# Kernel optimization log

Measured on AMD Instinct MI355X. Metric: run time of the kernel, lower is better.

The kernel has to match this reference:

```python
import jax, jax.numpy as jnp
import numpy as np

B, T = 1, 1024
HID = 2048
H, HKV, D = 16, 4, 128
G = H // HKV          # kv groups
TOPK = 256
HI, DI = 4, 32        # indexer heads / head dim


def _rotate_half(x):
    x1, x2 = jnp.split(x, 2, axis=-1)
    return jnp.concatenate([-x2, x1], axis=-1)


def _apply_rotary(x, cos, sin):
    # x: (B,T,H,D), cos/sin: (1,T,1,D)
    return x * cos + _rotate_half(x) * sin


def _rms_norm(x):
    eps = jnp.finfo(x.dtype).eps
    return x * jax.lax.rsqrt(jnp.mean(x * x, axis=-1, keepdims=True) + eps)


def setup_inputs() -> dict:
    key = jax.random.key(0)
    ks = jax.random.split(key, 9)
    s = 0.02
    x = jax.random.normal(ks[0], (B, T, HID), jnp.float32)
    # rotary tables
    inv_freq = 1.0 / (10000.0 ** (jnp.arange(0, D, 2, dtype=jnp.float32) / D))
    freqs = jnp.outer(jnp.arange(T, dtype=jnp.float32), inv_freq)   # (T, D/2)
    emb = jnp.concatenate([freqs, freqs], axis=-1)                  # (T, D)
    cos = jnp.cos(emb)[None, :, None, :]
    sin = jnp.sin(emb)[None, :, None, :]
    Wq = jax.random.normal(ks[1], (HID, H * D), jnp.float32) * s
    Wk = jax.random.normal(ks[2], (HID, HKV * D), jnp.float32) * s
    Wv = jax.random.normal(ks[3], (HID, HKV * D), jnp.float32) * s
    Wo = jax.random.normal(ks[4], (H * D, HID), jnp.float32) * s
    Wqi = jax.random.normal(ks[5], (HID, HI * DI), jnp.float32) * s
    Wwi = jax.random.normal(ks[6], (HID, HI), jnp.float32) * s
    Wki = jax.random.normal(ks[7], (HID, DI), jnp.float32) * s
    return {"x": x, "cos": cos, "sin": sin, "Wq": Wq, "Wk": Wk, "Wv": Wv,
            "Wo": Wo, "Wqi": Wqi, "Wwi": Wwi, "Wki": Wki}


def reference(x, cos, sin, Wq, Wk, Wv, Wo, Wqi, Wwi, Wki):
    b, t, _ = x.shape
    q = (x @ Wq).reshape(b, t, H, D)
    k = (x @ Wk).reshape(b, t, HKV, D)
    v = (x @ Wv).reshape(b, t, HKV, D)
    q = _rms_norm(_apply_rotary(q, cos, sin))
    k = _rms_norm(_apply_rotary(k, cos, sin))

    # ---- lightning indexer: I[t,s] = sum_j w[t,j] * relu(q_i[t,j] . k_i[s]) ----
    qi = (x @ Wqi).reshape(b, t, HI, DI)
    wi = x @ Wwi                                   # (B,T,HI)
    ki = x @ Wki                                   # (B,T,DI)
    raw = jax.nn.relu(jnp.einsum('bthd,bsd->bths', qi, ki))
    idx_scores = jnp.einsum('bths,bth->bts', raw, wi)     # (B,T,T)

    pos = jnp.arange(t)
    causal = pos[None, :] <= pos[:, None]                 # (T,T) valid s<=t
    masked = jnp.where(causal[None], idx_scores, -jnp.inf)
    _, top_idx = jax.lax.top_k(masked, TOPK)              # (B,T,K) int32

    # gather selected K/V: (B,T,K,HKV,D)
    gather = jax.vmap(lambda arr, idx: arr[idx])          # per-batch fancy gather
    sel_k = gather(k, top_idx)
    sel_v = gather(v, top_idx)
    sel_mask = top_idx <= pos[None, :, None]              # (B,T,K)

    # grouped-query attention over selected tokens (avoid repeat_interleave)
    q5 = q.reshape(b, t, HKV, G, D)                       # q head h -> kv head h//G
    scale = D ** -0.5
    scores = jnp.einsum('btngd,btknd->btngk', q5, sel_k) * scale
    scores = jnp.where(sel_mask[:, :, None, None, :], scores, -jnp.inf)
    probs = jax.nn.softmax(scores, axis=-1)
    attn = jnp.einsum('btngk,btknd->btngd', probs, sel_v)  # (B,T,HKV,G,D)
    out = attn.reshape(b, t, H * D) @ Wo
    return out
```

## Files before the change

kernel.cpp:

```cpp
#include <hip/hip_runtime.h>
#include <hip/hip_bf16.h>
#include <math.h>

#define T_    1024
#define HID_  2048
#define NH    16
#define NKV   4
#define DH    128
#define TOPK_ 256
#define HI_   4
#define DI_   32
#define NPROJ 3072
#define NIDX  164
#define KSPLIT 8
#define KCHUNK 256

#ifndef INFINITY
#define INFINITY (__builtin_inff())
#endif

typedef __attribute__((ext_vector_type(8))) short bf16x8;
typedef __attribute__((ext_vector_type(4))) float f32x4;

__device__ inline unsigned int packbf(float f) {
    unsigned int u = __float_as_uint(f);
    return (u + 0x7fffu + ((u >> 16) & 1u)) >> 16;
}

#define GLDS16(g, l) __builtin_amdgcn_global_load_lds( \
    (const __attribute__((address_space(1))) void*)(g), \
    (__attribute__((address_space(3))) void*)(l), 16, 0, 0)

__device__ inline void tcast_body(const float* __restrict__ W, unsigned short* __restrict__ Wt,
                                  int N, int bx, int by, int tid, float (*tile)[33]) {
    const int n0 = bx * 32, k0 = by * 32;
    const int tx = tid & 31, ty = tid >> 5;
#pragma unroll
    for (int i = 0; i < 4; ++i)
        tile[ty + i * 8][tx] = W[(size_t)(k0 + ty + i * 8) * N + (n0 + tx)];
    __syncthreads();
#pragma unroll
    for (int i = 0; i < 4; ++i) {
        int n = n0 + ty + i * 8;
        Wt[(size_t)n * HID_ + k0 + tx] = (unsigned short)packbf(tile[tx][ty + i * 8]);
    }
}

__global__ __launch_bounds__(256) void prep1(const float* __restrict__ x,
                                             const float* __restrict__ Wq,
                                             const float* __restrict__ Wk,
                                             const float* __restrict__ Wv,
                                             const float* __restrict__ Wqi,
                                             const float* __restrict__ Wwi,
                                             const float* __restrict__ Wki,
                                             unsigned short* __restrict__ xb,
                                             unsigned short* __restrict__ WtAll,
                                             float* __restrict__ Wi) {
    __shared__ float tile[32][33];
    int bid = blockIdx.x;
    const int tid = threadIdx.x;
    if (bid < 4096) { tcast_body(Wq, WtAll, HID_, bid & 63, bid >> 6, tid, tile); return; }
    bid -= 4096;
    if (bid < 1024) { tcast_body(Wk, WtAll + (size_t)2048 * HID_, 512, bid & 15, bid >> 4, tid, tile); return; }
    bid -= 1024;
    if (bid < 1024) { tcast_body(Wv, WtAll + (size_t)2560 * HID_, 512, bid & 15, bid >> 4, tid, tile); return; }
    bid -= 1024;
    if (bid < 1024) {
        int e = bid * 256 + tid;
        const float4* p = (const float4*)(x + (size_t)e * 8);
        float4 a = p[0], b = p[1];
        uint4 r;
        r.x = packbf(a.x) | (packbf(a.y) << 16);
        r.y = packbf(a.z) | (packbf(a.w) << 16);
        r.z = packbf(b.x) | (packbf(b.y) << 16);
        r.w = packbf(b.z) | (packbf(b.w) << 16);
        *(uint4*)(xb + (size_t)e * 8) = r;
        return;
    }
    bid -= 1024;
    {
        int e = bid * 256 + tid;
        if (e >= HID_ * NIDX) return;
        int k = e / NIDX, c = e - k * NIDX;
        float v;
        if (c < 128) v = Wqi[(size_t)k * 128 + c];
        else if (c < 132) v = Wwi[(size_t)k * 4 + (c - 128)];
        else v = Wki[(size_t)k * 32 + (c - 132)];
        Wi[e] = v;
    }
}

__global__ void tcast(const float* __restrict__ W, unsigned short* __restrict__ Wt, int N) {
    __shared__ float tile[32][33];
    const int n0 = blockIdx.x * 32, k0 = blockIdx.y * 32;
    const int tx = threadIdx.x, ty = threadIdx.y;
#pragma unroll
    for (int i = 0; i < 4; ++i)
        tile[ty + i * 8][tx] = W[(size_t)(k0 + ty + i * 8) * N + (n0 + tx)];
    __syncthreads();
#pragma unroll
    for (int i = 0; i < 4; ++i) {
        int n = n0 + ty + i * 8;
        Wt[(size_t)n * HID_ + k0 + tx] = (unsigned short)packbf(tile[tx][ty + i * 8]);
    }
}

__global__ __launch_bounds__(256) void gemm64(const unsigned short* __restrict__ A,
                                              const unsigned short* __restrict__ Bt,
                                              float* __restrict__ C,
                                              int K, int ldc) {
    __shared__ unsigned short As[64 * 64];
    __shared__ unsigned short Bs[64 * 64];
    const int tid = threadIdx.x, lane = tid & 63, w = tid >> 6;
    const int wr = w >> 1, wc = w & 1;
    const int brow = blockIdx.y * 64, bcol = blockIdx.x * 64;
    const int l15 = lane & 15, lq = lane >> 4;

    f32x4 acc[2][2] = {};

    const int srow = tid >> 3;
    const int gsrc = ((tid & 7) ^ (srow & 7)) * 8;
    const unsigned short* ga  = A  + (size_t)(brow + srow) * K + gsrc;
    const unsigned short* ga2 = ga + (size_t)32 * K;
    const unsigned short* gb  = Bt + (size_t)(bcol + srow) * K + gsrc;
    const unsigned short* gb2 = gb + (size_t)32 * K;
    unsigned short* la  = &As[(size_t)tid * 8];
    unsigned short* la2 = &As[(size_t)(tid + 256) * 8];
    unsigned short* lb  = &Bs[(size_t)tid * 8];
    unsigned short* lb2 = &Bs[(size_t)(tid + 256) * 8];

    for (int k0 = 0; k0 < K; k0 += 64) {
        GLDS16(ga + k0,  la);
        GLDS16(ga2 + k0, la2);
        GLDS16(gb + k0,  lb);
        GLDS16(gb2 + k0, lb2);
        __syncthreads();
        bf16x8 fa[2][2], fb[2][2];
#pragma unroll
        for (int m = 0; m < 2; ++m)
#pragma unroll
            for (int kk = 0; kk < 2; ++kk) {
                int row = wr * 32 + m * 16 + l15;
                fa[m][kk] = *(const bf16x8*)&As[row * 64 + (((kk * 4 + lq) ^ (l15 & 7)) * 8)];
            }
#pragma unroll
        for (int nn = 0; nn < 2; ++nn)
#pragma unroll
            for (int kk = 0; kk < 2; ++kk) {
                int row = wc * 32 + nn * 16 + l15;
                fb[nn][kk] = *(const bf16x8*)&Bs[row * 64 + (((kk * 4 + lq) ^ (l15 & 7)) * 8)];
            }
#pragma unroll
        for (int kk = 0; kk < 2; ++kk)
#pragma unroll
            for (int m = 0; m < 2; ++m)
#pragma unroll
                for (int nn = 0; nn < 2; ++nn)
                    acc[m][nn] = __builtin_amdgcn_mfma_f32_16x16x32_bf16(fa[m][kk], fb[nn][kk], acc[m][nn], 0, 0, 0);
        __syncthreads();
    }
#pragma unroll
    for (int m = 0; m < 2; ++m)
#pragma unroll
        for (int nn = 0; nn < 2; ++nn)
#pragma unroll
            for (int q = 0; q < 4; ++q) {
                int row = brow + wr * 32 + m * 16 + lq * 4 + q;
                int col = bcol + wc * 32 + nn * 16 + l15;
                C[(size_t)row * ldc + col] = acc[m][nn][q];
            }
}

__global__ void gemm_f32_splitk(const float* __restrict__ A, const float* __restrict__ B,
                                float* __restrict__ Cpart, int M, int N, int K) {
    __shared__ float As2[16][64 + 1];
    __shared__ float Bs2[16][64 + 1];
    const int tid = threadIdx.x;
    const int tx = tid & 15, ty = tid >> 4;
    const int brow = blockIdx.y * 64, bcol = blockIdx.x * 64;
    const int z = blockIdx.z;
    const int kbeg = z * KCHUNK, kend = kbeg + KCHUNK;

    float acc[4][4];
#pragma unroll
    for (int i = 0; i < 4; ++i)
#pragma unroll
        for (int j = 0; j < 4; ++j) acc[i][j] = 0.f;

    for (int k0 = kbeg; k0 < kend; k0 += 16) {
#pragma unroll
        for (int it = 0; it < 4; ++it) {
            int i = tid + it * 256;
            int r = i >> 4, c = i & 15;
            As2[c][r] = A[(size_t)(brow + r) * K + (k0 + c)];
        }
#pragma unroll
        for (int it = 0; it < 4; ++it) {
            int i = tid + it * 256;
            int r = i >> 6, c = i & 63;
            int col = bcol + c;
            Bs2[r][c] = (col < N) ? B[(size_t)(k0 + r) * N + col] : 0.f;
        }
        __syncthreads();
#pragma unroll
        for (int kk = 0; kk < 16; ++kk) {
            float a[4], b[4];
#pragma unroll
            for (int i = 0; i < 4; ++i) a[i] = As2[kk][ty * 4 + i];
#pragma unroll
            for (int j = 0; j < 4; ++j) b[j] = Bs2[kk][tx * 4 + j];
#pragma unroll
            for (int i = 0; i < 4; ++i)
#pragma unroll
                for (int j = 0; j < 4; ++j) acc[i][j] += a[i] * b[j];
        }
        __syncthreads();
    }
#pragma unroll
    for (int i = 0; i < 4; ++i) {
        int r = brow + ty * 4 + i;
#pragma unroll
        for (int j = 0; j < 4; ++j) {
            int c = bcol + tx * 4 + j;
            if (c < N) Cpart[((size_t)z * M + r) * N + c] = acc[i][j];
        }
    }
}

__global__ __launch_bounds__(256) void reduce_k(const float* __restrict__ Cpart,
                                                float* __restrict__ Cout,
                                                float* __restrict__ kib, int MN) {
    int e = blockIdx.x * 256 + threadIdx.x;
    if (e >= MN) return;
    float s = 0.f;
#pragma unroll
    for (int z = 0; z < KSPLIT; ++z) s += Cpart[(size_t)z * MN + e];
    Cout[e] = s;
    int t = e / NIDX, c = e - t * NIDX;
    if (c >= 132) kib[(size_t)t * DI_ + (c - 132)] = s;
}

__global__ void rope_fused(const float* __restrict__ proj, const float* __restrict__ cosb,
                           const float* __restrict__ sinb, unsigned short* __restrict__ qbb,
                           unsigned short* __restrict__ kbb, unsigned int* __restrict__ vbb) {
    const int t = blockIdx.x, h = blockIdx.y, lane = threadIdx.x;
    if (h < 20) {
        const float* row;
        unsigned short* dst;
        if (h < 16) { row = proj + (size_t)t * NPROJ + h * DH;           dst = qbb + ((size_t)t * NH + h) * DH; }
        else        { row = proj + (size_t)t * NPROJ + HID_ + (h - 16) * DH; dst = kbb + ((size_t)t * NKV + (h - 16)) * DH; }
        float a = row[lane], b = row[lane + 64];
        float c0 = cosb[t * DH + lane],      s0 = sinb[t * DH + lane];
        float c1 = cosb[t * DH + lane + 64], s1 = sinb[t * DH + lane + 64];
        float r0 = a * c0 - b * s0;
        float r1 = b * c1 + a * s1;
        float ss = r0 * r0 + r1 * r1;
#pragma unroll
        for (int o = 32; o > 0; o >>= 1) ss += __shfl_xor(ss, o);
        float inv = rsqrtf(ss * (1.0f / 128.0f) + 1.1920929e-07f);
        dst[lane]      = (unsigned short)packbf(r0 * inv);
        dst[lane + 64] = (unsigned short)packbf(r1 * inv);
    } else {
        const float* src = proj + (size_t)t * NPROJ + HID_ + 512;
#pragma unroll
        for (int i = 0; i < 4; ++i) {
            int c2 = lane + i * 64;
            vbb[(size_t)t * 256 + c2] = packbf(src[2 * c2]) | (packbf(src[2 * c2 + 1]) << 16);
        }
    }
}

__global__ __launch_bounds__(256) void idxtopk(const float* __restrict__ proji,
                                               const float* __restrict__ kib,
                                               int* __restrict__ idxout) {
    const int t = blockIdx.x, tid = threadIdx.x;
    int* orow = idxout + (size_t)t * TOPK_;
    if (t < TOPK_) { orow[tid] = tid; return; }

    __shared__ float qsh[128];
    __shared__ float wsh[4];
    if (tid < 128) qsh[tid] = proji[(size_t)t * NIDX + tid];
    else if (tid < 132) wsh[tid - 128] = proji[(size_t)t * NIDX + tid];
    __syncthreads();

    const int n = t + 1;
    const int lane = tid & 63, wave = tid >> 6;

    unsigned int key[4];
#pragma unroll
    for (int j = 0; j < 4; ++j) {
        int s = j * 256 + tid;
        if (s < n) {
            const float4* kr = (const float4*)&kib[(size_t)s * DI_];
            float4 k4[8];
#pragma unroll
            for (int d4 = 0; d4 < 8; ++d4) k4[d4] = kr[d4];
            float sc = 0.f;
#pragma unroll
            for (int h = 0; h < HI_; ++h) {
                float d = 0.f;
#pragma unroll
                for (int d4 = 0; d4 < 8; ++d4) {
                    const float* qp = &qsh[h * 32 + d4 * 4];
                    d += k4[d4].x * qp[0] + k4[d4].y * qp[1] +
                         k4[d4].z * qp[2] + k4[d4].w * qp[3];
                }
                sc += wsh[h] * fmaxf(d, 0.f);
            }
            unsigned int u = __float_as_uint(sc);
            key[j] = (u & 0x80000000u) ? ~u : (u | 0x80000000u);
        } else key[j] = 0u;
    }

    __shared__ int wcnt[2][4];
    unsigned int prefix = 0;
#pragma unroll 1
    for (int b = 31; b >= 0; --b) {
        unsigned int cand = prefix | (1u << b);
        int c = (key[0] >= cand) + (key[1] >= cand) + (key[2] >= cand) + (key[3] >= cand);
#pragma unroll
        for (int o = 32; o > 0; o >>= 1) c += __shfl_xor(c, o);
        if (lane == 0) wcnt[b & 1][wave] = c;
        __syncthreads();
        int total = wcnt[b & 1][0] + wcnt[b & 1][1] + wcnt[b & 1][2] + wcnt[b & 1][3];
        if (total >= TOPK_) prefix = cand;
    }
    const unsigned int T = prefix;

    __shared__ int posc;
    __shared__ int eqtot[4][4];
    __syncthreads();
    {
        int c = (key[0] > T) + (key[1] > T) + (key[2] > T) + (key[3] > T);
#pragma unroll
        for (int o = 32; o > 0; o >>= 1) c += __shfl_xor(c, o);
        if (lane == 0) wcnt[0][wave] = c;
    }
    if (tid == 0) posc = 0;

    int e[4]; int myp[4];
#pragma unroll
    for (int j = 0; j < 4; ++j) {
        e[j] = (key[j] == T) ? 1 : 0;
        unsigned long long m = __ballot(e[j]);
        myp[j] = __popcll(m & ((1ull << lane) - 1ull));
        if (lane == 0) eqtot[j][wave] = __popcll(m);
    }
    __syncthreads();
    const int cntGT = wcnt[0][0] + wcnt[0][1] + wcnt[0][2] + wcnt[0][3];
    const int need = TOPK_ - cntGT;

#pragma unroll
    for (int j = 0; j < 4; ++j)
        if (key[j] > T) {
            int p = atomicAdd(&posc, 1);
            orow[p] = j * 256 + tid;
        }
    int runbase = 0;
#pragma unroll
    for (int j = 0; j < 4; ++j) {
        int wavebase = 0;
#pragma unroll
        for (int w2 = 0; w2 < 4; ++w2) if (w2 < wave) wavebase += eqtot[j][w2];
        int g = runbase + wavebase + myp[j];
        if (e[j] && g < need) orow[cntGT + g] = j * 256 + tid;
        runbase += eqtot[j][0] + eqtot[j][1] + eqtot[j][2] + eqtot[j][3];
    }
}

__global__ __launch_bounds__(256) void attn3(const unsigned short* __restrict__ qbb,
                                             const unsigned short* __restrict__ kbb,
                                             const unsigned short* __restrict__ vbb,
                                             const int* __restrict__ idx,
                                             unsigned short* __restrict__ attnb) {
    const int t = blockIdx.x, n = blockIdx.y;
    const int tid = threadIdx.x, lane = tid & 63, w = tid >> 6;
    const int C = (t + 1 < TOPK_) ? t + 1 : TOPK_;
    const int l15 = lane & 15, lq = lane >> 4;

    __shared__ int sidx[TOPK_];
    __shared__ float sp[4][TOPK_];
    __shared__ float sinv[4];
    __shared__ unsigned short P[16][264];
    __shared__ unsigned short Vs[64][136];

    sidx[tid] = idx[(size_t)t * TOPK_ + tid];
    __syncthreads();

    const size_t qrow = (size_t)t * NH + n * 4 + (l15 < 4 ? l15 : 3);
    bf16x8 qf[4];
#pragma unroll
    for (int ks = 0; ks < 4; ++ks)
        qf[ks] = *(const bf16x8*)&qbb[qrow * DH + ks * 32 + lq * 8];

#pragma unroll
    for (int tt = 0; tt < 4; ++tt) {
        const int tile = w * 4 + tt;
        const int tok = tile * 16 + l15;
        const unsigned short* krow = &kbb[((size_t)sidx[tok] * NKV + n) * DH];
        f32x4 acc = {0.f, 0.f, 0.f, 0.f};
        __builtin_amdgcn_s_setprio(1);
#pragma unroll
        for (int ks = 0; ks < 4; ++ks) {
            bf16x8 yf = *(const bf16x8*)&krow[ks * 32 + lq * 8];
            acc = __builtin_amdgcn_mfma_f32_16x16x32_bf16(qf[ks], yf, acc, 0, 0, 0);
        }
        __builtin_amdgcn_s_setprio(0);
        if (lane < 16) {
            int j = tile * 16 + lane;
            bool ok = j < C;
#pragma unroll
            for (int q = 0; q < 4; ++q)
                sp[q][j] = ok ? acc[q] * 0.08838834764831845f : -INFINITY;
        }
    }
    __syncthreads();

    {
        float v0 = sp[w][lane], v1 = sp[w][lane + 64],
              v2 = sp[w][lane + 128], v3 = sp[w][lane + 192];
        float m = fmaxf(fmaxf(v0, v1), fmaxf(v2, v3));
#pragma unroll
        for (int o = 32; o > 0; o >>= 1) m = fmaxf(m, __shfl_xor(m, o));
        float e0 = expf(v0 - m), e1 = expf(v1 - m), e2 = expf(v2 - m), e3 = expf(v3 - m);
        float sum = e0 + e1 + e2 + e3;
#pragma unroll
        for (int o = 32; o > 0; o >>= 1) sum += __shfl_xor(sum, o);
        if (lane == 0) sinv[w] = 1.f / sum;
        P[w][lane]       = (unsigned short)packbf(e0);
        P[w][lane + 64]  = (unsigned short)packbf(e1);
        P[w][lane + 128] = (unsigned short)packbf(e2);
        P[w][lane + 192] = (unsigned short)packbf(e3);
    }

    f32x4 pacc[2] = {};
#pragma unroll 1
    for (int tau = 0; tau < 4; ++tau) {
        __syncthreads();
#pragma unroll
        for (int it = 0; it < 4; ++it) {
            int c = tid + it * 256;
            int r = c >> 4, doff = (c & 15) * 8;
            int col = doff ^ (((r >> 3) & 3) << 4);
            *(uint4*)&Vs[r][col] =
                *(const uint4*)&vbb[((size_t)sidx[tau * 64 + r] * NKV + n) * DH + doff];
        }
        __syncthreads();
#pragma unroll
        for (int kk = 0; kk < 2; ++kk) {
            bf16x8 xf = *(const bf16x8*)&P[l15][tau * 64 + kk * 32 + lq * 8];
            const int colr0 = ((2 * w + 0) * 16 + l15) ^ (lq << 4);
            const int colr1 = ((2 * w + 1) * 16 + l15) ^ (lq << 4);
            bf16x8 yf0, yf1;
#pragma unroll
            for (int j = 0; j < 8; ++j) {
                yf0[j] = (short)Vs[kk * 32 + lq * 8 + j][colr0];
                yf1[j] = (short)Vs[kk * 32 + lq * 8 + j][colr1];
            }
            __builtin_amdgcn_s_setprio(1);
            pacc[0] = __builtin_amdgcn_mfma_f32_16x16x32_bf16(xf, yf0, pacc[0], 0, 0, 0);
            pacc[1] = __builtin_amdgcn_mfma_f32_16x16x32_bf16(xf, yf1, pacc[1], 0, 0, 0);
            __builtin_amdgcn_s_setprio(0);
        }
    }

    if (lane < 16) {
#pragma unroll
        for (int dt = 0; dt < 2; ++dt)
#pragma unroll
            for (int q = 0; q < 4; ++q)
                attnb[(size_t)(t * NH + n * 4 + q) * DH + (2 * w + dt) * 16 + l15] =
                    (unsigned short)packbf(pacc[dt][q] * sinv[q]);
    }
}

extern "C" void kernel_launch(void* const* d_in, const int* in_sizes, int n_in,
                              void* d_out, int out_size, void* d_ws, size_t ws_size,
                              hipStream_t stream) {
    const float* x    = (const float*)d_in[0];
    const float* cosb = (const float*)d_in[1];
    const float* sinb = (const float*)d_in[2];
    const float* Wq   = (const float*)d_in[3];
    const float* Wk   = (const float*)d_in[4];
    const float* Wv   = (const float*)d_in[5];
    const float* Wo   = (const float*)d_in[6];
    const float* Wqi  = (const float*)d_in[7];
    const float* Wwi  = (const float*)d_in[8];
    const float* Wki  = (const float*)d_in[9];
    float* out = (float*)d_out;

    unsigned short* xb    = (unsigned short*)d_ws;
    unsigned short* WtAll = xb + 2097152;
    float*  proj  = (float*)(WtAll + 6291456);
    float*  Wi    = proj + 3145728;
    float*  proji = Wi + 335872;
    float*  kib   = proji + 167936;
    int*    idxb  = (int*)(kib + 1048576);
    unsigned short* kbb   = (unsigned short*)(idxb + 262144);
    unsigned short* vbb   = kbb + 524288;
    unsigned short* attnb = vbb + 524288;
    unsigned short* Wot   = WtAll;
    unsigned short* qbb   = xb;
    float* Cpart = (float*)kbb;

    prep1<<<dim3(8480), dim3(256), 0, stream>>>(x, Wq, Wk, Wv, Wqi, Wwi, Wki, xb, WtAll, Wi);

    gemm64<<<dim3(NPROJ / 64, T_ / 64), dim3(256), 0, stream>>>(xb, WtAll, proj, HID_, NPROJ);
    gemm_f32_splitk<<<dim3((NIDX + 63) / 64, T_ / 64, KSPLIT), dim3(256), 0, stream>>>(x, Wi, Cpart, T_, NIDX, HID_);
    reduce_k<<<dim3((T_ * NIDX + 255) / 256), dim3(256), 0, stream>>>(Cpart, proji, kib, T_ * NIDX);

    tcast<<<dim3(64, 64), dim3(32, 8), 0, stream>>>(Wo, Wot, HID_);

    rope_fused<<<dim3(T_, 21), dim3(64), 0, stream>>>(proj, cosb, sinb, qbb, kbb, (unsigned int*)vbb);

    idxtopk<<<dim3(T_), dim3(256), 0, stream>>>(proji, kib, idxb);

    attn3<<<dim3(T_, NKV), dim3(256), 0, stream>>>(qbb, kbb, vbb, idxb, attnb);

    gemm64<<<dim3(HID_ / 64, T_ / 64), dim3(256), 0, stream>>>(attnb, Wot, out, HID_, HID_);
}
```

Measured before the change: 183.7 us.

## Merge independent kernels into two heterogeneous block-dispatched launches

Combines the bf16 projection GEMM and the fp32 split-K indexer GEMM into one launch that picks its role from the block id. It also merges the RoPE/RMSnorm conversion, the Wo transpose-cast and the indexer top-k into a second launch. This removes several kernel launches and lets independent work fill the GPU at the same time. In exchange, blocks with very different resource needs share one kernel, so shared-memory size and register use are the union of all branches, which may reduce occupancy. RoPE now packs four tokens-heads per 256-thread block.

After: 183.9 us. About the same (+0.1%).

```diff
diff --git a/kernel.cpp b/kernel.cpp
--- a/kernel.cpp
+++ b/kernel.cpp
@@ -44,6 +44,71 @@
         int n = n0 + ty + i * 8;
         Wt[(size_t)n * HID_ + k0 + tx] = (unsigned short)packbf(tile[tx][ty + i * 8]);
     }
+}
+
+__device__ inline void gemm64_body(const unsigned short* __restrict__ A,
+                                   const unsigned short* __restrict__ Bt,
+                                   float* __restrict__ C, int K, int ldc,
+                                   int bx, int by, int tid,
+                                   unsigned short* As, unsigned short* Bs) {
+    const int lane = tid & 63, w = tid >> 6;
+    const int wr = w >> 1, wc = w & 1;
+    const int brow = by * 64, bcol = bx * 64;
+    const int l15 = lane & 15, lq = lane >> 4;
+
+    f32x4 acc[2][2] = {};
+
+    const int srow = tid >> 3;
+    const int gsrc = ((tid & 7) ^ (srow & 7)) * 8;
+    const unsigned short* ga  = A  + (size_t)(brow + srow) * K + gsrc;
+    const unsigned short* ga2 = ga + (size_t)32 * K;
+    const unsigned short* gb  = Bt + (size_t)(bcol + srow) * K + gsrc;
+    const unsigned short* gb2 = gb + (size_t)32 * K;
+    unsigned short* la  = &As[(size_t)tid * 8];
+    unsigned short* la2 = &As[(size_t)(tid + 256) * 8];
+    unsigned short* lb  = &Bs[(size_t)tid * 8];
+    unsigned short* lb2 = &Bs[(size_t)(tid + 256) * 8];
+
+    for (int k0 = 0; k0 < K; k0 += 64) {
+        GLDS16(ga + k0,  la);
+        GLDS16(ga2 + k0, la2);
+        GLDS16(gb + k0,  lb);
+        GLDS16(gb2 + k0, lb2);
+        __syncthreads();
+        bf16x8 fa[2][2], fb[2][2];
+#pragma unroll
+        for (int m = 0; m < 2; ++m)
+#pragma unroll
+            for (int kk = 0; kk < 2; ++kk) {
+                int row = wr * 32 + m * 16 + l15;
+                fa[m][kk] = *(const bf16x8*)&As[row * 64 + (((kk * 4 + lq) ^ (l15 & 7)) * 8)];
+            }
+#pragma unroll
+        for (int nn = 0; nn < 2; ++nn)
+#pragma unroll
+            for (int kk = 0; kk < 2; ++kk) {
+                int row = wc * 32 + nn * 16 + l15;
+                fb[nn][kk] = *(const bf16x8*)&Bs[row * 64 + (((kk * 4 + lq) ^ (l15 & 7)) * 8)];
+            }
+#pragma unroll
+        for (int kk = 0; kk < 2; ++kk)
+#pragma unroll
+            for (int m = 0; m < 2; ++m)
+#pragma unroll
+                for (int nn = 0; nn < 2; ++nn)
+                    acc[m][nn] = __builtin_amdgcn_mfma_f32_16x16x32_bf16(fa[m][kk], fb[nn][kk], acc[m][nn], 0, 0, 0);
+        __syncthreads();
+    }
+#pragma unroll
+    for (int m = 0; m < 2; ++m)
+#pragma unroll
+        for (int nn = 0; nn < 2; ++nn)
+#pragma unroll
+            for (int q = 0; q < 4; ++q) {
+                int row = brow + wr * 32 + m * 16 + lq * 4 + q;
+                int col = bcol + wc * 32 + nn * 16 + l15;
+                C[(size_t)row * ldc + col] = acc[m][nn][q];
+            }
 }
 
 __global__ __launch_bounds__(256) void prep1(const float* __restrict__ x,
@@ -90,18 +155,234 @@
     }
 }
 
-__global__ void tcast(const float* __restrict__ W, unsigned short* __restrict__ Wt, int N) {
+__global__ __launch_bounds__(256) void fusedA(const unsigned short* __restrict__ xb,
+                                              const unsigned short* __restrict__ WtAll,
+                                              float* __restrict__ proj,
+                                              const float* __restrict__ x,
+                                              const float* __restrict__ Wi,
+                                              float* __restrict__ Cpart) {
+    __shared__ unsigned short As[64 * 64];
+    __shared__ unsigned short Bs[64 * 64];
+    __shared__ float As2[16][64 + 1];
+    __shared__ float Bs2[16][64 + 1];
+    const int tid = threadIdx.x;
+    int bid = blockIdx.x;
+
+    if (bid < 768) {
+        gemm64_body(xb, WtAll, proj, HID_, NPROJ, bid % 48, bid / 48, tid, As, Bs);
+        return;
+    }
+    int s = bid - 768;
+    const int bx = s % 3, by = (s / 3) % 16, z = s / 48;
+    const int tx = tid & 15, ty = tid >> 4;
+    const int brow = by * 64, bcol = bx * 64;
+    const int kbeg = z * KCHUNK, kend = kbeg + KCHUNK;
+    const int M = T_, N = NIDX, K = HID_;
+
+    float acc[4][4];
+#pragma unroll
+    for (int i = 0; i < 4; ++i)
+#pragma unroll
+        for (int j = 0; j < 4; ++j) acc[i][j] = 0.f;
+
+    for (int k0 = kbeg; k0 < kend; k0 += 16) {
+#pragma unroll
+        for (int it = 0; it < 4; ++it) {
+            int i = tid + it * 256;
+            int r = i >> 4, c = i & 15;
+            As2[c][r] = x[(size_t)(brow + r) * K + (k0 + c)];
+        }
+#pragma unroll
+        for (int it = 0; it < 4; ++it) {
+            int i = tid + it * 256;
+            int r = i >> 6, c = i & 63;
+            int col = bcol + c;
+            Bs2[r][c] = (col < N) ? Wi[(size_t)(k0 + r) * N + col] : 0.f;
+        }
+        __syncthreads();
+#pragma unroll
+        for (int kk = 0; kk < 16; ++kk) {
+            float a[4], b[4];
+#pragma unroll
+            for (int i = 0; i < 4; ++i) a[i] = As2[kk][ty * 4 + i];
+#pragma unroll
+            for (int j = 0; j < 4; ++j) b[j] = Bs2[kk][tx * 4 + j];
+#pragma unroll
+            for (int i = 0; i < 4; ++i)
+#pragma unroll
+                for (int j = 0; j < 4; ++j) acc[i][j] += a[i] * b[j];
+        }
+        __syncthreads();
+    }
+#pragma unroll
+    for (int i = 0; i < 4; ++i) {
+        int r = brow + ty * 4 + i;
+#pragma unroll
+        for (int j = 0; j < 4; ++j) {
+            int c = bcol + tx * 4 + j;
+            if (c < N) Cpart[((size_t)z * M + r) * N + c] = acc[i][j];
+        }
+    }
+}
+
+__global__ __launch_bounds__(256) void reduce_k(const float* __restrict__ Cpart,
+                                                float* __restrict__ Cout,
+                                                float* __restrict__ kib, int MN) {
+    int e = blockIdx.x * 256 + threadIdx.x;
+    if (e >= MN) return;
+    float s = 0.f;
+#pragma unroll
+    for (int z = 0; z < KSPLIT; ++z) s += Cpart[(size_t)z * MN + e];
+    Cout[e] = s;
+    int t = e / NIDX, c = e - t * NIDX;
+    if (c >= 132) kib[(size_t)t * DI_ + (c - 132)] = s;
+}
+
+__global__ __launch_bounds__(256) void fusedB(const float* __restrict__ proj,
+                                              const float* __restrict__ cosb,
+                                              const float* __restrict__ sinb,
+                                              unsigned short* __restrict__ qbb,
+                                              unsigned short* __restrict__ kbb,
+                                              unsigned int* __restrict__ vbb,
+                                              const float* __restrict__ Wo,
+                                              unsigned short* __restrict__ Wot,
+                                              const float* __restrict__ proji,
+                                              const float* __restrict__ kib,
+                                              int* __restrict__ idxout) {
     __shared__ float tile[32][33];
-    const int n0 = blockIdx.x * 32, k0 = blockIdx.y * 32;
-    const int tx = threadIdx.x, ty = threadIdx.y;
-#pragma unroll
-    for (int i = 0; i < 4; ++i)
-        tile[ty + i * 8][tx] = W[(size_t)(k0 + ty + i * 8) * N + (n0 + tx)];
-    __syncthreads();
-#pragma unroll
-    for (int i = 0; i < 4; ++i) {
-        int n = n0 + ty + i * 8;
-        Wt[(size_t)n * HID_ + k0 + tx] = (unsigned short)packbf(tile[tx][ty + i * 8]);
+    const int tid = threadIdx.x;
+    int bid = blockIdx.x;
+
+    if (bid < 5376) {
+        const int w = tid >> 6, lane = tid & 63;
+        const int u = bid * 4 + w;
+        const int t = u / 21, h = u - t * 21;
+        if (h < 20) {
+            const float* row;
+            unsigned short* dst;
+            if (h < 16) { row = proj + (size_t)t * NPROJ + h * DH;               dst = qbb + ((size_t)t * NH + h) * DH; }
+            else        { row = proj + (size_t)t * NPROJ + HID_ + (h - 16) * DH; dst = kbb + ((size_t)t * NKV + (h - 16)) * DH; }
+            float a = row[lane], b = row[lane + 64];
+            float c0 = cosb[t * DH + lane],      s0 = sinb[t * DH + lane];
+            float c1 = cosb[t * DH + lane + 64], s1 = sinb[t * DH + lane + 64];
+            float r0 = a * c0 - b * s0;
+            float r1 = b * c1 + a * s1;
+            float ss = r0 * r0 + r1 * r1;
+#pragma unroll
+            for (int o = 32; o > 0; o >>= 1) ss += __shfl_xor(ss, o);
+            float inv = rsqrtf(ss * (1.0f / 128.0f) + 1.1920929e-07f);
+            dst[lane]      = (unsigned short)packbf(r0 * inv);
+            dst[lane + 64] = (unsigned short)packbf(r1 * inv);
+        } else {
+            const float* src = proj + (size_t)t * NPROJ + HID_ + 512;
+#pragma unroll
+            for (int i = 0; i < 4; ++i) {
+                int c2 = lane + i * 64;
+                vbb[(size_t)t * 256 + c2] = packbf(src[2 * c2]) | (packbf(src[2 * c2 + 1]) << 16);
+            }
+        }
+        return;
+    }
+    bid -= 5376;
+    if (bid < 4096) {
+        tcast_body(Wo, Wot, HID_, bid & 63, bid >> 6, tid, tile);
+        return;
+    }
+    bid -= 4096;
+    {
+        const int t = bid;
+        int* orow = idxout + (size_t)t * TOPK_;
+        if (t < TOPK_) { orow[tid] = tid; return; }
+
+        __shared__ float qsh[128];
+        __shared__ float wsh[4];
+        if (tid < 128) qsh[tid] = proji[(size_t)t * NIDX + tid];
+        else if (tid < 132) wsh[tid - 128] = proji[(size_t)t * NIDX + tid];
+        __syncthreads();
+
+        const int n = t + 1;
+        const int lane = tid & 63, wave = tid >> 6;
+
+        unsigned int key[4];
+#pragma unroll
+        for (int j = 0; j < 4; ++j) {
+            int s = j * 256 + tid;
+            if (s < n) {
+                const float4* kr = (const float4*)&kib[(size_t)s * DI_];
+                float4 k4[8];
+#pragma unroll
+                for (int d4 = 0; d4 < 8; ++d4) k4[d4] = kr[d4];
+                float sc = 0.f;
+#pragma unroll
+                for (int h = 0; h < HI_; ++h) {
+                    float d = 0.f;
+#pragma unroll
+                    for (int d4 = 0; d4 < 8; ++d4) {
+                        const float* qp = &qsh[h * 32 + d4 * 4];
+                        d += k4[d4].x * qp[0] + k4[d4].y * qp[1] +
+                             k4[d4].z * qp[2] + k4[d4].w * qp[3];
+                    }
+                    sc += wsh[h] * fmaxf(d, 0.f);
+                }
+                unsigned int u = __float_as_uint(sc);
+                key[j] = (u & 0x80000000u) ? ~u : (u | 0x80000000u);
+            } else key[j] = 0u;
+        }
+
+        __shared__ int wcnt[2][4];
+        unsigned int prefix = 0;
+#pragma unroll 1
+        for (int b = 31; b >= 0; --b) {
+            unsigned int cand = prefix | (1u << b);
+            int c = (key[0] >= cand) + (key[1] >= cand) + (key[2] >= cand) + (key[3] >= cand);
+#pragma unroll
+            for (int o = 32; o > 0; o >>= 1) c += __shfl_xor(c, o);
+            if (lane == 0) wcnt[b & 1][wave] = c;
+            __syncthreads();
+            int total = wcnt[b & 1][0] + wcnt[b & 1][1] + wcnt[b & 1][2] + wcnt[b & 1][3];
+            if (total >= TOPK_) prefix = cand;
+        }
+        const unsigned int T = prefix;
+
+        __shared__ int posc;
+        __shared__ int eqtot[4][4];
+        __syncthreads();
+        {
+            int c = (key[0] > T) + (key[1] > T) + (key[2] > T) + (key[3] > T);
+#pragma unroll
+            for (int o = 32; o > 0; o >>= 1) c += __shfl_xor(c, o);
+            if (lane == 0) wcnt[0][wave] = c;
+        }
+        if (tid == 0) posc = 0;
+
+        int e[4]; int myp[4];
+#pragma unroll
+        for (int j = 0; j < 4; ++j) {
+            e[j] = (key[j] == T) ? 1 : 0;
+            unsigned long long m = __ballot(e[j]);
+            myp[j] = __popcll(m & ((1ull << lane) - 1ull));
+            if (lane == 0) eqtot[j][wave] = __popcll(m);
+        }
+        __syncthreads();
+        const int cntGT = wcnt[0][0] + wcnt[0][1] + wcnt[0][2] + wcnt[0][3];
+        const int need = TOPK_ - cntGT;
+
+#pragma unroll
+        for (int j = 0; j < 4; ++j)
+            if (key[j] > T) {
+                int p = atomicAdd(&posc, 1);
+                orow[p] = j * 256 + tid;
+            }
+        int runbase = 0;
+#pragma unroll
+        for (int j = 0; j < 4; ++j) {
+            int wavebase = 0;
+#pragma unroll
+            for (int w2 = 0; w2 < 4; ++w2) if (w2 < wave) wavebase += eqtot[j][w2];
+            int g = runbase + wavebase + myp[j];
+            if (e[j] && g < need) orow[cntGT + g] = j * 256 + tid;
+            runbase += eqtot[j][0] + eqtot[j][1] + eqtot[j][2] + eqtot[j][3];
+        }
     }
 }
 
@@ -111,261 +392,7 @@
                                               int K, int ldc) {
     __shared__ unsigned short As[64 * 64];
     __shared__ unsigned short Bs[64 * 64];
-    const int tid = threadIdx.x, lane = tid & 63, w = tid >> 6;
-    const int wr = w >> 1, wc = w & 1;
-    const int brow = blockIdx.y * 64, bcol = blockIdx.x * 64;
-    const int l15 = lane & 15, lq = lane >> 4;
-
-    f32x4 acc[2][2] = {};
-
-    const int srow = tid >> 3;
-    const int gsrc = ((tid & 7) ^ (srow & 7)) * 8;
-    const unsigned short* ga  = A  + (size_t)(brow + srow) * K + gsrc;
-    const unsigned short* ga2 = ga + (size_t)32 * K;
-    const unsigned short* gb  = Bt + (size_t)(bcol + srow) * K + gsrc;
-    const unsigned short* gb2 = gb + (size_t)32 * K;
-    unsigned short* la  = &As[(size_t)tid * 8];
-    unsigned short* la2 = &As[(size_t)(tid + 256) * 8];
-    unsigned short* lb  = &Bs[(size_t)tid * 8];
-    unsigned short* lb2 = &Bs[(size_t)(tid + 256) * 8];
-
-    for (int k0 = 0; k0 < K; k0 += 64) {
-        GLDS16(ga + k0,  la);
-        GLDS16(ga2 + k0, la2);
-        GLDS16(gb + k0,  lb);
-        GLDS16(gb2 + k0, lb2);
-        __syncthreads();
-        bf16x8 fa[2][2], fb[2][2];
-#pragma unroll
-        for (int m = 0; m < 2; ++m)
-#pragma unroll
-            for (int kk = 0; kk < 2; ++kk) {
-                int row = wr * 32 + m * 16 + l15;
-                fa[m][kk] = *(const bf16x8*)&As[row * 64 + (((kk * 4 + lq) ^ (l15 & 7)) * 8)];
-            }
-#pragma unroll
-        for (int nn = 0; nn < 2; ++nn)
-#pragma unroll
-            for (int kk = 0; kk < 2; ++kk) {
-                int row = wc * 32 + nn * 16 + l15;
-                fb[nn][kk] = *(const bf16x8*)&Bs[row * 64 + (((kk * 4 + lq) ^ (l15 & 7)) * 8)];
-            }
-#pragma unroll
-        for (int kk = 0; kk < 2; ++kk)
-#pragma unroll
-            for (int m = 0; m < 2; ++m)
-#pragma unroll
-                for (int nn = 0; nn < 2; ++nn)
-                    acc[m][nn] = __builtin_amdgcn_mfma_f32_16x16x32_bf16(fa[m][kk], fb[nn][kk], acc[m][nn], 0, 0, 0);
-        __syncthreads();
-    }
-#pragma unroll
-    for (int m = 0; m < 2; ++m)
-#pragma unroll
-        for (int nn = 0; nn < 2; ++nn)
-#pragma unroll
-            for (int q = 0; q < 4; ++q) {
-                int row = brow + wr * 32 + m * 16 + lq * 4 + q;
-                int col = bcol + wc * 32 + nn * 16 + l15;
-                C[(size_t)row * ldc + col] = acc[m][nn][q];
-            }
-}
-
-__global__ void gemm_f32_splitk(const float* __restrict__ A, const float* __restrict__ B,
-                                float* __restrict__ Cpart, int M, int N, int K) {
-    __shared__ float As2[16][64 + 1];
-    __shared__ float Bs2[16][64 + 1];
-    const int tid = threadIdx.x;
-    const int tx = tid & 15, ty = tid >> 4;
-    const int brow = blockIdx.y * 64, bcol = blockIdx.x * 64;
-    const int z = blockIdx.z;
-    const int kbeg = z * KCHUNK, kend = kbeg + KCHUNK;
-
-    float acc[4][4];
-#pragma unroll
-    for (int i = 0; i < 4; ++i)
-#pragma unroll
-        for (int j = 0; j < 4; ++j) acc[i][j] = 0.f;
-
-    for (int k0 = kbeg; k0 < kend; k0 += 16) {
-#pragma unroll
-        for (int it = 0; it < 4; ++it) {
-            int i = tid + it * 256;
-            int r = i >> 4, c = i & 15;
-            As2[c][r] = A[(size_t)(brow + r) * K + (k0 + c)];
-        }
-#pragma unroll
-        for (int it = 0; it < 4; ++it) {
-            int i = tid + it * 256;
-            int r = i >> 6, c = i & 63;
-            int col = bcol + c;
-            Bs2[r][c] = (col < N) ? B[(size_t)(k0 + r) * N + col] : 0.f;
-        }
-        __syncthreads();
-#pragma unroll
-        for (int kk = 0; kk < 16; ++kk) {
-            float a[4], b[4];
-#pragma unroll
-            for (int i = 0; i < 4; ++i) a[i] = As2[kk][ty * 4 + i];
-#pragma unroll
-            for (int j = 0; j < 4; ++j) b[j] = Bs2[kk][tx * 4 + j];
-#pragma unroll
-            for (int i = 0; i < 4; ++i)
-#pragma unroll
-                for (int j = 0; j < 4; ++j) acc[i][j] += a[i] * b[j];
-        }
-        __syncthreads();
-    }
-#pragma unroll
-    for (int i = 0; i < 4; ++i) {
-        int r = brow + ty * 4 + i;
-#pragma unroll
-        for (int j = 0; j < 4; ++j) {
-            int c = bcol + tx * 4 + j;
-            if (c < N) Cpart[((size_t)z * M + r) * N + c] = acc[i][j];
-        }
-    }
-}
-
-__global__ __launch_bounds__(256) void reduce_k(const float* __restrict__ Cpart,
-                                                float* __restrict__ Cout,
-                                                float* __restrict__ kib, int MN) {
-    int e = blockIdx.x * 256 + threadIdx.x;
-    if (e >= MN) return;
-    float s = 0.f;
-#pragma unroll
-    for (int z = 0; z < KSPLIT; ++z) s += Cpart[(size_t)z * MN + e];
-    Cout[e] = s;
-    int t = e / NIDX, c = e - t * NIDX;
-    if (c >= 132) kib[(size_t)t * DI_ + (c - 132)] = s;
-}
-
-__global__ void rope_fused(const float* __restrict__ proj, const float* __restrict__ cosb,
-                           const float* __restrict__ sinb, unsigned short* __restrict__ qbb,
-                           unsigned short* __restrict__ kbb, unsigned int* __restrict__ vbb) {
-    const int t = blockIdx.x, h = blockIdx.y, lane = threadIdx.x;
-    if (h < 20) {
-        const float* row;
-        unsigned short* dst;
-        if (h < 16) { row = proj + (size_t)t * NPROJ + h * DH;           dst = qbb + ((size_t)t * NH + h) * DH; }
-        else        { row = proj + (size_t)t * NPROJ + HID_ + (h - 16) * DH; dst = kbb + ((size_t)t * NKV + (h - 16)) * DH; }
-        float a = row[lane], b = row[lane + 64];
-        float c0 = cosb[t * DH + lane],      s0 = sinb[t * DH + lane];
-        float c1 = cosb[t * DH + lane + 64], s1 = sinb[t * DH + lane + 64];
-        float r0 = a * c0 - b * s0;
-        float r1 = b * c1 + a * s1;
-        float ss = r0 * r0 + r1 * r1;
-#pragma unroll
-        for (int o = 32; o > 0; o >>= 1) ss += __shfl_xor(ss, o);
-        float inv = rsqrtf(ss * (1.0f / 128.0f) + 1.1920929e-07f);
-        dst[lane]      = (unsigned short)packbf(r0 * inv);
-        dst[lane + 64] = (unsigned short)packbf(r1 * inv);
-    } else {
-        const float* src = proj + (size_t)t * NPROJ + HID_ + 512;
-#pragma unroll
-        for (int i = 0; i < 4; ++i) {
-            int c2 = lane + i * 64;
-            vbb[(size_t)t * 256 + c2] = packbf(src[2 * c2]) | (packbf(src[2 * c2 + 1]) << 16);
-        }
-    }
-}
-
-__global__ __launch_bounds__(256) void idxtopk(const float* __restrict__ proji,
-                                               const float* __restrict__ kib,
-                                               int* __restrict__ idxout) {
-    const int t = blockIdx.x, tid = threadIdx.x;
-    int* orow = idxout + (size_t)t * TOPK_;
-    if (t < TOPK_) { orow[tid] = tid; return; }
-
-    __shared__ float qsh[128];
-    __shared__ float wsh[4];
-    if (tid < 128) qsh[tid] = proji[(size_t)t * NIDX + tid];
-    else if (tid < 132) wsh[tid - 128] = proji[(size_t)t * NIDX + tid];
-    __syncthreads();
-
-    const int n = t + 1;
-    const int lane = tid & 63, wave = tid >> 6;
-
-    unsigned int key[4];
-#pragma unroll
-    for (int j = 0; j < 4; ++j) {
-        int s = j * 256 + tid;
-        if (s < n) {
-            const float4* kr = (const float4*)&kib[(size_t)s * DI_];
-            float4 k4[8];
-#pragma unroll
-            for (int d4 = 0; d4 < 8; ++d4) k4[d4] = kr[d4];
-            float sc = 0.f;
-#pragma unroll
-            for (int h = 0; h < HI_; ++h) {
-                float d = 0.f;
-#pragma unroll
-                for (int d4 = 0; d4 < 8; ++d4) {
-                    const float* qp = &qsh[h * 32 + d4 * 4];
-                    d += k4[d4].x * qp[0] + k4[d4].y * qp[1] +
-                         k4[d4].z * qp[2] + k4[d4].w * qp[3];
-                }
-                sc += wsh[h] * fmaxf(d, 0.f);
-            }
-            unsigned int u = __float_as_uint(sc);
-            key[j] = (u & 0x80000000u) ? ~u : (u | 0x80000000u);
-        } else key[j] = 0u;
-    }
-
-    __shared__ int wcnt[2][4];
-    unsigned int prefix = 0;
-#pragma unroll 1
-    for (int b = 31; b >= 0; --b) {
-        unsigned int cand = prefix | (1u << b);
-        int c = (key[0] >= cand) + (key[1] >= cand) + (key[2] >= cand) + (key[3] >= cand);
-#pragma unroll
-        for (int o = 32; o > 0; o >>= 1) c += __shfl_xor(c, o);
-        if (lane == 0) wcnt[b & 1][wave] = c;
-        __syncthreads();
-        int total = wcnt[b & 1][0] + wcnt[b & 1][1] + wcnt[b & 1][2] + wcnt[b & 1][3];
-        if (total >= TOPK_) prefix = cand;
-    }
-    const unsigned int T = prefix;
-
-    __shared__ int posc;
-    __shared__ int eqtot[4][4];
-    __syncthreads();
-    {
-        int c = (key[0] > T) + (key[1] > T) + (key[2] > T) + (key[3] > T);
-#pragma unroll
-        for (int o = 32; o > 0; o >>= 1) c += __shfl_xor(c, o);
-        if (lane == 0) wcnt[0][wave] = c;
-    }
-    if (tid == 0) posc = 0;
-
-    int e[4]; int myp[4];
-#pragma unroll
-    for (int j = 0; j < 4; ++j) {
-        e[j] = (key[j] == T) ? 1 : 0;
-        unsigned long long m = __ballot(e[j]);
-        myp[j] = __popcll(m & ((1ull << lane) - 1ull));
-        if (lane == 0) eqtot[j][wave] = __popcll(m);
-    }
-    __syncthreads();
-    const int cntGT = wcnt[0][0] + wcnt[0][1] + wcnt[0][2] + wcnt[0][3];
-    const int need = TOPK_ - cntGT;
-
-#pragma unroll
-    for (int j = 0; j < 4; ++j)
-        if (key[j] > T) {
-            int p = atomicAdd(&posc, 1);
-            orow[p] = j * 256 + tid;
-        }
-    int runbase = 0;
-#pragma unroll
-    for (int j = 0; j < 4; ++j) {
-        int wavebase = 0;
-#pragma unroll
-        for (int w2 = 0; w2 < 4; ++w2) if (w2 < wave) wavebase += eqtot[j][w2];
-        int g = runbase + wavebase + myp[j];
-        if (e[j] && g < need) orow[cntGT + g] = j * 256 + tid;
-        runbase += eqtot[j][0] + eqtot[j][1] + eqtot[j][2] + eqtot[j][3];
-    }
+    gemm64_body(A, Bt, C, K, ldc, blockIdx.x, blockIdx.y, threadIdx.x, As, Bs);
 }
 
 __global__ __launch_bounds__(256) void attn3(const unsigned short* __restrict__ qbb,
@@ -505,15 +532,12 @@
 
     prep1<<<dim3(8480), dim3(256), 0, stream>>>(x, Wq, Wk, Wv, Wqi, Wwi, Wki, xb, WtAll, Wi);
 
-    gemm64<<<dim3(NPROJ / 64, T_ / 64), dim3(256), 0, stream>>>(xb, WtAll, proj, HID_, NPROJ);
-    gemm_f32_splitk<<<dim3((NIDX + 63) / 64, T_ / 64, KSPLIT), dim3(256), 0, stream>>>(x, Wi, Cpart, T_, NIDX, HID_);
+    fusedA<<<dim3(1152), dim3(256), 0, stream>>>(xb, WtAll, proj, x, Wi, Cpart);
+
     reduce_k<<<dim3((T_ * NIDX + 255) / 256), dim3(256), 0, stream>>>(Cpart, proji, kib, T_ * NIDX);
 
-    tcast<<<dim3(64, 64), dim3(32, 8), 0, stream>>>(Wo, Wot, HID_);
-
-    rope_fused<<<dim3(T_, 21), dim3(64), 0, stream>>>(proj, cosb, sinb, qbb, kbb, (unsigned int*)vbb);
-
-    idxtopk<<<dim3(T_), dim3(256), 0, stream>>>(proji, kib, idxb);
+    fusedB<<<dim3(10496), dim3(256), 0, stream>>>(proj, cosb, sinb, qbb, kbb, (unsigned int*)vbb,
+                                                  Wo, Wot, proji, kib, idxb);
 
     attn3<<<dim3(T_, NKV), dim3(256), 0, stream>>>(qbb, kbb, vbb, idxb, attnb);
 
```
